# Performance work log

Hardware: AMD Instinct MI355X
Metric: run time of the kernel (lower is better)

Reference implementation:

```python
import jax, jax.numpy as jnp
import numpy as np

B, S, D, H = 32, 1024, 256, 256


def setup_inputs() -> dict:
    key = jax.random.key(0)
    ks = jax.random.split(key, 7)
    s_in = 1.0 / np.sqrt(D)
    s_h = 1.0 / np.sqrt(H)
    x = jax.random.normal(ks[0], (B, S, D), dtype=jnp.float32)
    # gate order: i, f, g, o stacked along last dim -> 4H
    W_fwd = jax.random.uniform(ks[1], (D, 4 * H), dtype=jnp.float32, minval=-s_in, maxval=s_in)
    U_fwd = jax.random.uniform(ks[2], (H, 4 * H), dtype=jnp.float32, minval=-s_h, maxval=s_h)
    b_fwd = jax.random.uniform(ks[3], (4 * H,), dtype=jnp.float32, minval=-s_in, maxval=s_in)
    W_rev = jax.random.uniform(ks[4], (D, 4 * H), dtype=jnp.float32, minval=-s_in, maxval=s_in)
    U_rev = jax.random.uniform(ks[5], (H, 4 * H), dtype=jnp.float32, minval=-s_h, maxval=s_h)
    b_rev = jax.random.uniform(ks[6], (4 * H,), dtype=jnp.float32, minval=-s_in, maxval=s_in)
    return {"x": x, "W_fwd": W_fwd, "U_fwd": U_fwd, "b_fwd": b_fwd,
            "W_rev": W_rev, "U_rev": U_rev, "b_rev": b_rev}


def _lstm_scan(x, W, U, b):
    # x: [B, S, D] -> outputs h over time: [B, S, H]
    hdim = U.shape[0]
    # precompute input projection for all steps: [S, B, 4H]
    xW = jnp.einsum('bsd,dg->sbg', x, W) + b

    def step(carry, xw_t):
        h, c = carry
        gates = xw_t + h @ U  # [B, 4H]
        i_t = jax.nn.sigmoid(gates[:, 0 * hdim:1 * hdim])
        f_t = jax.nn.sigmoid(gates[:, 1 * hdim:2 * hdim])
        g_t = jnp.tanh(gates[:, 2 * hdim:3 * hdim])
        o_t = jax.nn.sigmoid(gates[:, 3 * hdim:4 * hdim])
        c_t = f_t * c + i_t * g_t
        h_t = o_t * jnp.tanh(c_t)
        return (h_t, c_t), h_t

    bsz = x.shape[0]
    h0 = jnp.zeros((bsz, hdim), dtype=x.dtype)
    c0 = jnp.zeros((bsz, hdim), dtype=x.dtype)
    _, hs = jax.lax.scan(step, (h0, c0), xW)
    return jnp.transpose(hs, (1, 0, 2))  # [B, S, H]


def reference(x, W_fwd, U_fwd, b_fwd, W_rev, U_rev, b_rev):
    out_f = _lstm_scan(x, W_fwd, U_fwd, b_fwd)
    out_r = _lstm_scan(x[:, ::-1, :], W_rev, U_rev, b_rev)[:, ::-1, :]
    return jnp.concatenate([out_f, out_r], axis=2)  # [B, S, 2H]
```

## Files before the change

kernel.cpp:

```cpp
#include <hip/hip_runtime.h>
#include <hip/hip_bf16.h>

typedef _Float16 f16;
typedef _Float16 half8 __attribute__((ext_vector_type(8)));
typedef float f32x4 __attribute__((ext_vector_type(4)));
typedef int i32x4 __attribute__((ext_vector_type(4)));


__global__ void prep_uq_kernel(const float* __restrict__ Uf, const float* __restrict__ Ur,
                               unsigned int* __restrict__ UQm, float* __restrict__ Uscale)
{
    int idx = blockIdx.x * 256 + threadIdx.x;
    if (idx >= 2048) return;
    int dir = idx >> 10, c = idx & 1023;
    const float* U = dir ? Ur : Uf;
    float m = 0.f;
    for (int k = 0; k < 256; ++k) m = fmaxf(m, fabsf(U[k * 1024 + c]));
    float sinv = (m > 0.f) ? 127.f / m : 0.f;
    int tile = c >> 4, colr = c & 15;
    uint4* UQm4 = (uint4*)UQm;
    for (int ks = 0; ks < 4; ++ks) {
        #pragma unroll
        for (int kg = 0; kg < 4; ++kg) {
            unsigned int w[4];
            #pragma unroll
            for (int d = 0; d < 4; ++d) {
                unsigned int wd = 0;
                #pragma unroll
                for (int e = 0; e < 4; ++e) {
                    int k = ks * 64 + kg * 16 + d * 4 + e;
                    int q = __float2int_rn(U[k * 1024 + c] * sinv);
                    wd |= ((unsigned int)(q & 0xff)) << (8 * e);
                }
                w[d] = wd;
            }
            UQm4[((size_t)((dir * 64 + tile) * 4 + ks)) * 64 + kg * 16 + colr] =
                make_uint4(w[0], w[1], w[2], w[3]);
        }
    }
    Uscale[idx] = m / (127.f * 127.f);
}

__global__ __launch_bounds__(256) void proj_gemm_kernel(
    const float* __restrict__ x, const float* __restrict__ Wf, const float* __restrict__ Wr,
    const float* __restrict__ bfw, const float* __restrict__ brw, f16* __restrict__ G)
{
    const int nt = blockIdx.x;
    const int mt = blockIdx.y;
    const int m0 = mt * 128, n0 = nt * 128;
    const int dir = n0 >> 10, nin0 = n0 & 1023;
    const float* W   = dir ? Wr : Wf;
    const float* bia = dir ? brw : bfw;
    __shared__ f16 Asm[128][40];
    __shared__ f16 Bsm[128][40];
    const int t = threadIdx.x;
    const int lane = t & 63, wave = t >> 6;
    const int wr = wave >> 1, wc = wave & 1;
    f32x4 acc[4][4] = {};
    for (int k0 = 0; k0 < 256; k0 += 32) {
        #pragma unroll
        for (int e = 0; e < 16; ++e) {
            int idx = e * 256 + t;
            int r = idx >> 5, kk = idx & 31;
            Asm[r][kk] = (f16)x[(size_t)(m0 + r) * 256 + (k0 + kk)];
        }
        #pragma unroll
        for (int e = 0; e < 16; ++e) {
            int idx = e * 256 + t;
            int col = idx & 127, kr = idx >> 7;
            Bsm[col][kr] = (f16)W[(size_t)(k0 + kr) * 1024 + (nin0 + col)];
        }
        __syncthreads();
        const int l15 = lane & 15, kb = (lane >> 4) * 8;
        half8 af[4], bfr[4];
        #pragma unroll
        for (int fr = 0; fr < 4; ++fr) af[fr]  = *(const half8*)&Asm[wr * 64 + fr * 16 + l15][kb];
        #pragma unroll
        for (int fc = 0; fc < 4; ++fc) bfr[fc] = *(const half8*)&Bsm[wc * 64 + fc * 16 + l15][kb];
        #pragma unroll
        for (int fr = 0; fr < 4; ++fr)
            #pragma unroll
            for (int fc = 0; fc < 4; ++fc)
                acc[fr][fc] = __builtin_amdgcn_mfma_f32_16x16x32_f16(af[fr], bfr[fc], acc[fr][fc], 0, 0, 0);
        __syncthreads();
    }
    const int row4 = (lane >> 4) * 4, c15 = lane & 15;
    #pragma unroll
    for (int fr = 0; fr < 4; ++fr)
        #pragma unroll
        for (int fc = 0; fc < 4; ++fc) {
            int rbase = m0 + wr * 64 + fr * 16 + row4;
            int cidx  = n0 + wc * 64 + fc * 16 + c15;
            float bv = bia[cidx & 1023];
            #pragma unroll
            for (int i = 0; i < 4; ++i)
                G[(size_t)(rbase + i) * 2048 + cidx] = (f16)(acc[fr][fc][i] + bv);
        }
}

template<int PAT>
__device__ __forceinline__ float qb(float v) {
    return __int_as_float(__builtin_amdgcn_mov_dpp(__float_as_int(v), PAT, 0xF, 0xF, true));
}

#define LGKM_BARRIER() do { \
    asm volatile("s_waitcnt lgkmcnt(0)\n\ts_barrier" ::: "memory"); \
    __builtin_amdgcn_sched_barrier(0); \
} while (0)

__global__
__attribute__((amdgpu_flat_work_group_size(1024, 1024)))
__attribute__((amdgpu_waves_per_eu(4, 4)))
void scan_kernel(
    const f16* __restrict__ G, const unsigned int* __restrict__ UQm,
    const float* __restrict__ Uscale, float* __restrict__ out)
{
    const int wg = blockIdx.x;
    const int dir = wg >> 5, b = wg & 31;
    const int tid = threadIdx.x;
    const int wave = tid >> 6, lane = tid & 63;
    const int colq = lane >> 2, gate = lane & 3;
    const int mycol = wave * 16 + colq;

    __shared__ __align__(16) unsigned int hq[128];
    __shared__ __align__(16) int scr[1024];

    if (tid < 64) hq[tid] = 0u;

    const i32x4* UQm4 = (const i32x4*)UQm;
    i32x4 uf0[4], uf1[4], uf2[4], uf3[4];
    #pragma unroll
    for (int ks = 0; ks < 4; ++ks) {
        uf0[ks] = UQm4[((size_t)((dir * 64 + ( 0 + wave)) * 4 + ks)) * 64 + lane];
        uf1[ks] = UQm4[((size_t)((dir * 64 + (16 + wave)) * 4 + ks)) * 64 + lane];
        uf2[ks] = UQm4[((size_t)((dir * 64 + (32 + wave)) * 4 + ks)) * 64 + lane];
        uf3[ks] = UQm4[((size_t)((dir * 64 + (48 + wave)) * 4 + ks)) * 64 + lane];
    }

    const float uscl = Uscale[dir * 1024 + gate * 256 + mycol];

    const f16* Gl = G + (size_t)b * 1024 * 2048 + dir * 1024 + gate * 256 + mycol;
    float* outp = out + (size_t)b * 1024 * 512 + dir * 256 + mycol;

    const int s0 = dir ? 1023 : 0;
    float xw = (float)Gl[(size_t)s0 * 2048];
    float c_state = 0.f;
    __syncthreads();

    const char* hqb = (const char*)hq;
    signed char* hqw = (signed char*)hq;
    int* scrw = scr + wave * 64;
    const int arow = (lane >> 4) << 4;
    int p = 0;

    for (int t = 0; t < 1024; ++t) {
        const int s  = dir ? (1023 - t) : t;
        const int tn = (t < 1023) ? (t + 1) : t;
        const int sn = dir ? (1023 - tn) : tn;
        f16 xn = Gl[(size_t)sn * 2048];

        i32x4 acc0 = {0,0,0,0}, acc1 = {0,0,0,0}, acc2 = {0,0,0,0}, acc3 = {0,0,0,0};
        #pragma unroll
        for (int ks = 0; ks < 4; ++ks) {
            i32x4 a = *(const i32x4*)(hqb + p * 256 + ks * 64 + arow);
            acc0 = __builtin_amdgcn_mfma_i32_16x16x64_i8(a, uf0[ks], acc0, 0, 0, 0);
            acc1 = __builtin_amdgcn_mfma_i32_16x16x64_i8(a, uf1[ks], acc1, 0, 0, 0);
            acc2 = __builtin_amdgcn_mfma_i32_16x16x64_i8(a, uf2[ks], acc2, 0, 0, 0);
            acc3 = __builtin_amdgcn_mfma_i32_16x16x64_i8(a, uf3[ks], acc3, 0, 0, 0);
        }

        if (lane < 16) {
            i32x4 pv; pv[0] = acc0[0]; pv[1] = acc1[0]; pv[2] = acc2[0]; pv[3] = acc3[0];
            *(i32x4*)(scrw + lane * 4) = pv;
        }
        asm volatile("s_waitcnt lgkmcnt(0)" ::: "memory");
        __builtin_amdgcn_sched_barrier(0);

        int iv = scrw[colq * 4 + gate];
        float pre = (float)iv * uscl + xw;
        float a2 = (gate == 2) ? (pre + pre) : -pre;
        float E  = __expf(a2);
        float r  = __fdividef(1.f, E + 1.f);
        float v  = (gate == 2) ? (1.f - 2.f * r) : r;
        float b0 = qb<0x00>(v), b1 = qb<0x55>(v), b2 = qb<0xAA>(v), b3 = qb<0xFF>(v);
        c_state = b1 * c_state + b0 * b2;
        float e2 = __expf(c_state + c_state);
        float th = 1.f - __fdividef(2.f, e2 + 1.f);
        float h  = b3 * th;

        if (gate == 0) outp[(size_t)s * 512] = h;
        if (gate == 1) hqw[(p ^ 1) * 256 + mycol] = (signed char)__float2int_rn(h * 127.f);

        LGKM_BARRIER();
        p ^= 1;
        xw = (float)xn;
    }
}

extern "C" void kernel_launch(void* const* d_in, const int* in_sizes, int n_in,
                              void* d_out, int out_size, void* d_ws, size_t ws_size,
                              hipStream_t stream) {
    const float* x  = (const float*)d_in[0];
    const float* Wf = (const float*)d_in[1];
    const float* Uf = (const float*)d_in[2];
    const float* bf = (const float*)d_in[3];
    const float* Wr = (const float*)d_in[4];
    const float* Ur = (const float*)d_in[5];
    const float* br = (const float*)d_in[6];
    float* out = (float*)d_out;

    char* ws = (char*)d_ws;
    unsigned int* UQm = (unsigned int*)ws;
    float* Uscale     = (float*)(ws + (size_t)512 * 1024);
    f16* G            = (f16*)(ws + (size_t)1024 * 1024);

    prep_uq_kernel<<<8, 256, 0, stream>>>(Uf, Ur, UQm, Uscale);
    dim3 gg(16, 256);
    proj_gemm_kernel<<<gg, 256, 0, stream>>>(x, Wf, Wr, bf, br, G);
    scan_kernel<<<64, 1024, 0, stream>>>(G, UQm, Uscale, out);
}
```

Baseline: 1.080 ms.

## Split recurrent matvec between MFMA waves and sdot4 VALU waves

The recurrent h@U product is split across the workgroup. Half the hidden columns (waves 0-7) still use int8 MFMA with weights held in registers. The other half (waves 8-15) compute per-lane int8 dot products with sdot4, reading h from LDS and weights preloaded into registers. A new weight layout is added for the dot-product waves. The aim is to halve the MFMA work per wave on the serial critical path and to use the VALU, at the cost of 64 sdot4 ops plus extra LDS reads per step on the VALU waves and possible wave imbalance.

Result: slower. 3.207 ms (+196.9%).

```diff
diff --git a/kernel.cpp b/kernel.cpp
--- a/kernel.cpp
+++ b/kernel.cpp
@@ -8,7 +8,8 @@
 
 
 __global__ void prep_uq_kernel(const float* __restrict__ Uf, const float* __restrict__ Ur,
-                               unsigned int* __restrict__ UQm, float* __restrict__ Uscale)
+                               unsigned int* __restrict__ UQm, unsigned int* __restrict__ UQd,
+                               float* __restrict__ Uscale)
 {
     int idx = blockIdx.x * 256 + threadIdx.x;
     if (idx >= 2048) return;
@@ -17,25 +18,39 @@
     float m = 0.f;
     for (int k = 0; k < 256; ++k) m = fmaxf(m, fabsf(U[k * 1024 + c]));
     float sinv = (m > 0.f) ? 127.f / m : 0.f;
-    int tile = c >> 4, colr = c & 15;
-    uint4* UQm4 = (uint4*)UQm;
-    for (int ks = 0; ks < 4; ++ks) {
-        #pragma unroll
-        for (int kg = 0; kg < 4; ++kg) {
-            unsigned int w[4];
-            #pragma unroll
-            for (int d = 0; d < 4; ++d) {
-                unsigned int wd = 0;
+    int g = c >> 8, hc = c & 255;
+    if (hc < 128) {
+        int w = hc >> 4, colr = hc & 15, mt = g * 8 + w;
+        uint4* UQm4 = (uint4*)UQm;
+        for (int ks = 0; ks < 4; ++ks) {
+            #pragma unroll
+            for (int kg = 0; kg < 4; ++kg) {
+                unsigned int wv[4];
                 #pragma unroll
-                for (int e = 0; e < 4; ++e) {
-                    int k = ks * 64 + kg * 16 + d * 4 + e;
-                    int q = __float2int_rn(U[k * 1024 + c] * sinv);
-                    wd |= ((unsigned int)(q & 0xff)) << (8 * e);
+                for (int d = 0; d < 4; ++d) {
+                    unsigned int wd = 0;
+                    #pragma unroll
+                    for (int e = 0; e < 4; ++e) {
+                        int k = ks * 64 + kg * 16 + d * 4 + e;
+                        int q = __float2int_rn(U[k * 1024 + c] * sinv);
+                        wd |= ((unsigned int)(q & 0xff)) << (8 * e);
+                    }
+                    wv[d] = wd;
                 }
-                w[d] = wd;
-            }
-            UQm4[((size_t)((dir * 64 + tile) * 4 + ks)) * 64 + kg * 16 + colr] =
-                make_uint4(w[0], w[1], w[2], w[3]);
+                UQm4[((size_t)((dir * 32 + mt) * 4 + ks)) * 64 + kg * 16 + colr] =
+                    make_uint4(wv[0], wv[1], wv[2], wv[3]);
+            }
+        }
+    } else {
+        int cc = g * 128 + (hc - 128);
+        for (int kk = 0; kk < 64; ++kk) {
+            unsigned int wd = 0;
+            #pragma unroll
+            for (int e = 0; e < 4; ++e) {
+                int q = __float2int_rn(U[(kk * 4 + e) * 1024 + c] * sinv);
+                wd |= ((unsigned int)(q & 0xff)) << (8 * e);
+            }
+            UQd[((size_t)(dir * 512 + cc)) * 64 + kk] = wd;
         }
     }
     Uscale[idx] = m / (127.f * 127.f);
@@ -98,6 +113,18 @@
         }
 }
 
+__device__ __forceinline__ int dot4i8(unsigned int a, unsigned int b, int c) {
+#if __has_builtin(__builtin_amdgcn_sdot4)
+    return __builtin_amdgcn_sdot4(a, b, c, false);
+#else
+    c += (int)(signed char)(a)       * (int)(signed char)(b);
+    c += (int)(signed char)(a >> 8)  * (int)(signed char)(b >> 8);
+    c += (int)(signed char)(a >> 16) * (int)(signed char)(b >> 16);
+    c += (int)(signed char)(a >> 24) * (int)(signed char)(b >> 24);
+    return c;
+#endif
+}
+
 template<int PAT>
 __device__ __forceinline__ float qb(float v) {
     return __int_as_float(__builtin_amdgcn_mov_dpp(__float_as_int(v), PAT, 0xF, 0xF, true));
@@ -113,35 +140,48 @@
 __attribute__((amdgpu_waves_per_eu(4, 4)))
 void scan_kernel(
     const f16* __restrict__ G, const unsigned int* __restrict__ UQm,
-    const float* __restrict__ Uscale, float* __restrict__ out)
+    const unsigned int* __restrict__ UQd, const float* __restrict__ Uscale,
+    float* __restrict__ out)
 {
     const int wg = blockIdx.x;
     const int dir = wg >> 5, b = wg & 31;
     const int tid = threadIdx.x;
     const int wave = tid >> 6, lane = tid & 63;
+    const bool mfma_w = (wave < 8);
     const int colq = lane >> 2, gate = lane & 3;
-    const int mycol = wave * 16 + colq;
+    const int hc = mfma_w ? (wave * 16 + colq) : (128 + (wave - 8) * 16 + colq);
 
     __shared__ __align__(16) unsigned int hq[128];
-    __shared__ __align__(16) int scr[1024];
+    __shared__ __align__(16) int scr[512];
 
     if (tid < 64) hq[tid] = 0u;
 
-    const i32x4* UQm4 = (const i32x4*)UQm;
     i32x4 uf0[4], uf1[4], uf2[4], uf3[4];
-    #pragma unroll
-    for (int ks = 0; ks < 4; ++ks) {
-        uf0[ks] = UQm4[((size_t)((dir * 64 + ( 0 + wave)) * 4 + ks)) * 64 + lane];
-        uf1[ks] = UQm4[((size_t)((dir * 64 + (16 + wave)) * 4 + ks)) * 64 + lane];
-        uf2[ks] = UQm4[((size_t)((dir * 64 + (32 + wave)) * 4 + ks)) * 64 + lane];
-        uf3[ks] = UQm4[((size_t)((dir * 64 + (48 + wave)) * 4 + ks)) * 64 + lane];
-    }
-
-    const float uscl = Uscale[dir * 1024 + gate * 256 + mycol];
-
-    const f16* Gl = G + (size_t)b * 1024 * 2048 + dir * 1024 + gate * 256 + mycol;
-    float* outp = out + (size_t)b * 1024 * 512 + dir * 256 + mycol;
-
+    uint4 ureg[16];
+    if (mfma_w) {
+        const i32x4* UQm4 = (const i32x4*)UQm;
+        #pragma unroll
+        for (int ks = 0; ks < 4; ++ks) {
+            uf0[ks] = UQm4[((size_t)((dir * 32 + ( 0 + wave)) * 4 + ks)) * 64 + lane];
+            uf1[ks] = UQm4[((size_t)((dir * 32 + ( 8 + wave)) * 4 + ks)) * 64 + lane];
+            uf2[ks] = UQm4[((size_t)((dir * 32 + (16 + wave)) * 4 + ks)) * 64 + lane];
+            uf3[ks] = UQm4[((size_t)((dir * 32 + (24 + wave)) * 4 + ks)) * 64 + lane];
+        }
+    } else {
+        const int cc = gate * 128 + (wave - 8) * 16 + colq;
+        const uint4* up = (const uint4*)(UQd + ((size_t)(dir * 512 + cc)) * 64);
+        #pragma unroll
+        for (int kkk = 0; kkk < 16; ++kkk)
+            asm volatile("global_load_dwordx4 %0, %1, off offset:%2"
+                         : "=v"(ureg[kkk]) : "v"(up), "i"(kkk * 16));
+        asm volatile("s_waitcnt vmcnt(0)" ::: "memory");
+        __builtin_amdgcn_sched_barrier(0);
+    }
+
+    const float uscl = Uscale[dir * 1024 + gate * 256 + hc];
+
+    const f16* Gl = G + (size_t)b * 1024 * 2048 + dir * 1024 + gate * 256 + hc;
+    float* outp = out + (size_t)b * 1024 * 512 + dir * 256 + hc;
     const int s0 = dir ? 1023 : 0;
     float xw = (float)Gl[(size_t)s0 * 2048];
     float c_state = 0.f;
@@ -149,7 +189,7 @@
 
     const char* hqb = (const char*)hq;
     signed char* hqw = (signed char*)hq;
-    int* scrw = scr + wave * 64;
+    int* scrw = scr + (mfma_w ? wave * 64 : 0);
     const int arow = (lane >> 4) << 4;
     int p = 0;
 
@@ -159,25 +199,54 @@
         const int sn = dir ? (1023 - tn) : tn;
         f16 xn = Gl[(size_t)sn * 2048];
 
-        i32x4 acc0 = {0,0,0,0}, acc1 = {0,0,0,0}, acc2 = {0,0,0,0}, acc3 = {0,0,0,0};
-        #pragma unroll
-        for (int ks = 0; ks < 4; ++ks) {
-            i32x4 a = *(const i32x4*)(hqb + p * 256 + ks * 64 + arow);
-            acc0 = __builtin_amdgcn_mfma_i32_16x16x64_i8(a, uf0[ks], acc0, 0, 0, 0);
-            acc1 = __builtin_amdgcn_mfma_i32_16x16x64_i8(a, uf1[ks], acc1, 0, 0, 0);
-            acc2 = __builtin_amdgcn_mfma_i32_16x16x64_i8(a, uf2[ks], acc2, 0, 0, 0);
-            acc3 = __builtin_amdgcn_mfma_i32_16x16x64_i8(a, uf3[ks], acc3, 0, 0, 0);
-        }
-
-        if (lane < 16) {
-            i32x4 pv; pv[0] = acc0[0]; pv[1] = acc1[0]; pv[2] = acc2[0]; pv[3] = acc3[0];
-            *(i32x4*)(scrw + lane * 4) = pv;
-        }
-        asm volatile("s_waitcnt lgkmcnt(0)" ::: "memory");
-        __builtin_amdgcn_sched_barrier(0);
-
-        int iv = scrw[colq * 4 + gate];
-        float pre = (float)iv * uscl + xw;
+        float pre;
+        if (mfma_w) {
+            i32x4 acc0 = {0,0,0,0}, acc1 = {0,0,0,0}, acc2 = {0,0,0,0}, acc3 = {0,0,0,0};
+            #pragma unroll
+            for (int ks = 0; ks < 4; ++ks) {
+                i32x4 a = *(const i32x4*)(hqb + p * 256 + ks * 64 + arow);
+                acc0 = __builtin_amdgcn_mfma_i32_16x16x64_i8(a, uf0[ks], acc0, 0, 0, 0);
+                acc1 = __builtin_amdgcn_mfma_i32_16x16x64_i8(a, uf1[ks], acc1, 0, 0, 0);
+                acc2 = __builtin_amdgcn_mfma_i32_16x16x64_i8(a, uf2[ks], acc2, 0, 0, 0);
+                acc3 = __builtin_amdgcn_mfma_i32_16x16x64_i8(a, uf3[ks], acc3, 0, 0, 0);
+            }
+            if (lane < 16) {
+                i32x4 pv; pv[0] = acc0[0]; pv[1] = acc1[0]; pv[2] = acc2[0]; pv[3] = acc3[0];
+                *(i32x4*)(scrw + lane * 4) = pv;
+            }
+            asm volatile("s_waitcnt lgkmcnt(0)" ::: "memory");
+            __builtin_amdgcn_sched_barrier(0);
+            pre = (float)scrw[colq * 4 + gate] * uscl + xw;
+        } else {
+            const uint4* hp4 = (const uint4*)(hqb + p * 256);
+            int i0 = 0, i1 = 0, i2 = 0, i3 = 0;
+            #pragma unroll
+            for (int ch = 0; ch < 4; ++ch) {
+                uint4 ha = hp4[ch * 4 + 0];
+                uint4 hb = hp4[ch * 4 + 1];
+                uint4 hc4 = hp4[ch * 4 + 2];
+                uint4 hd = hp4[ch * 4 + 3];
+                i0 = dot4i8(ureg[ch * 4 + 0].x, ha.x, i0);
+                i1 = dot4i8(ureg[ch * 4 + 0].y, ha.y, i1);
+                i2 = dot4i8(ureg[ch * 4 + 0].z, ha.z, i2);
+                i3 = dot4i8(ureg[ch * 4 + 0].w, ha.w, i3);
+                i0 = dot4i8(ureg[ch * 4 + 1].x, hb.x, i0);
+                i1 = dot4i8(ureg[ch * 4 + 1].y, hb.y, i1);
+                i2 = dot4i8(ureg[ch * 4 + 1].z, hb.z, i2);
+                i3 = dot4i8(ureg[ch * 4 + 1].w, hb.w, i3);
+                i0 = dot4i8(ureg[ch * 4 + 2].x, hc4.x, i0);
+                i1 = dot4i8(ureg[ch * 4 + 2].y, hc4.y, i1);
+                i2 = dot4i8(ureg[ch * 4 + 2].z, hc4.z, i2);
+                i3 = dot4i8(ureg[ch * 4 + 2].w, hc4.w, i3);
+                i0 = dot4i8(ureg[ch * 4 + 3].x, hd.x, i0);
+                i1 = dot4i8(ureg[ch * 4 + 3].y, hd.y, i1);
+                i2 = dot4i8(ureg[ch * 4 + 3].z, hd.z, i2);
+                i3 = dot4i8(ureg[ch * 4 + 3].w, hd.w, i3);
+                __builtin_amdgcn_sched_barrier(0);
+            }
+            pre = (float)((i0 + i1) + (i2 + i3)) * uscl + xw;
+        }
+
         float a2 = (gate == 2) ? (pre + pre) : -pre;
         float E  = __expf(a2);
         float r  = __fdividef(1.f, E + 1.f);
@@ -189,7 +258,7 @@
         float h  = b3 * th;
 
         if (gate == 0) outp[(size_t)s * 512] = h;
-        if (gate == 1) hqw[(p ^ 1) * 256 + mycol] = (signed char)__float2int_rn(h * 127.f);
+        if (gate == 1) hqw[(p ^ 1) * 256 + hc] = (signed char)__float2int_rn(h * 127.f);
 
         LGKM_BARRIER();
         p ^= 1;
@@ -211,11 +280,12 @@
 
     char* ws = (char*)d_ws;
     unsigned int* UQm = (unsigned int*)ws;
+    unsigned int* UQd = (unsigned int*)(ws + (size_t)256 * 1024);
     float* Uscale     = (float*)(ws + (size_t)512 * 1024);
     f16* G            = (f16*)(ws + (size_t)1024 * 1024);
 
-    prep_uq_kernel<<<8, 256, 0, stream>>>(Uf, Ur, UQm, Uscale);
+    prep_uq_kernel<<<8, 256, 0, stream>>>(Uf, Ur, UQm, UQd, Uscale);
     dim3 gg(16, 256);
     proj_gemm_kernel<<<gg, 256, 0, stream>>>(x, Wf, Wr, bf, br, G);
-    scan_kernel<<<64, 1024, 0, stream>>>(G, UQm, Uscale, out);
-}
+    scan_kernel<<<64, 1024, 0, stream>>>(G, UQm, UQd, Uscale, out);
+}
```
